# Kernel tuning notes

Hardware: AMD Instinct MI355X
Metric: run time of the kernel (lower is better)

Reference implementation:

```python
import jax, jax.numpy as jnp
import numpy as np

B, S, T, K = 96, 4, 16, 36           # groups, fixed 4 slots, max tags per slot, num boxes
V_DIM, Q_DIM, H = 1024, 512, 512


def setup_inputs() -> dict:
    key = jax.random.key(0)
    k_v, k_q, k_m, k_w1, k_b1, k_w2, k_b2 = jax.random.split(key, 7)

    # deterministic ragged lengths in [1, T], cyclic -> sum is exact
    lengths = (np.arange(B * S) % T) + 1              # [B*S], sum = 24 * 136 = 3264
    N = int(lengths.sum())                            # total rows in v / q
    # binary tag-attention mask: first `len` positions set per slot
    tags_attention = (np.arange(T)[None, :] < lengths[:, None]).astype(np.int32)
    tags_attention = jnp.asarray(tags_attention.reshape(B, S, T))

    v = jax.random.normal(k_v, (N, K, V_DIM), dtype=jnp.float32)
    q = jax.random.normal(k_q, (N, Q_DIM), dtype=jnp.float32)

    # box mask: random 0/1 but guarantee at least one valid box per group
    box_mask = (jax.random.uniform(k_m, (B, K)) < 0.9).astype(jnp.float32)
    box_mask = box_mask.at[:, 0].set(1.0)

    # FCNet (weight-normed Linear + ReLU; dropout inactive at eval) and scoring Linear
    w1 = jax.random.normal(k_w1, (V_DIM + Q_DIM, H), dtype=jnp.float32) * 0.02
    b1 = jax.random.normal(k_b1, (H,), dtype=jnp.float32) * 0.02
    w2 = jax.random.normal(k_w2, (H,), dtype=jnp.float32) * 0.02
    b2 = jax.random.normal(k_b2, (), dtype=jnp.float32) * 0.02

    return {"v": v, "q": q, "box_mask": box_mask, "tags_attention": tags_attention,
            "w1": w1, "b1": b1, "w2": w2, "b2": b2}


def reference(v, q, box_mask, tags_attention, w1, b1, w2, b2):
    N, Kb, _ = v.shape
    # logits: concat(v, q repeated over boxes) -> ReLU FC -> scalar score per box
    vq = jnp.concatenate([v, jnp.broadcast_to(q[:, None, :], (N, Kb, q.shape[-1]))], axis=-1)
    joint = jax.nn.relu(jnp.einsum('nkd,dh->nkh', vq, w1) + b1)      # [N, K, H]
    logits = jnp.einsum('nkh,h->nk', joint, w2) + b2                 # [N, K]

    # pad_sequence: ragged rows -> [B, S, T, K] via vectorized gather
    Bg, Sg, Tg = tags_attention.shape
    lengths = tags_attention.sum(-1).reshape(-1)                     # [B*S]
    starts = jnp.cumsum(lengths) - lengths                           # exclusive cumsum
    idx = starts[:, None] + jnp.arange(Tg)                           # [B*S, T]
    valid = jnp.arange(Tg)[None, :] < lengths[:, None]               # [B*S, T]
    gathered = jnp.take(logits, jnp.clip(idx, 0, N - 1), axis=0)     # [B*S, T, K]
    padded = jnp.where(valid[..., None], gathered, 0.0).reshape(Bg, Sg, Tg, Kb)

    # masked_softmax (allennlp-style) over the box dim with box_mask [B,1,1,K]
    mask = box_mask[:, None, None, :]
    s = jax.nn.softmax(padded * mask, axis=-1) * mask
    w = s / (s.sum(axis=-1, keepdims=True) + 1e-13)
    return w
```

## Files before the change

### kernel.cpp

```cpp
#include <hip/hip_runtime.h>
#include <hip/hip_bf16.h>
#include <cstdint>
#include <cstddef>

#define BB 96
#define SS 4
#define TT 16
#define KK 36
#define VDIM 1024
#define QDIM 512
#define HH 512
#define W1R 1536
#define NROWS 3264
#define MM (NROWS * KK)

typedef __attribute__((ext_vector_type(8))) short short8;
typedef __attribute__((ext_vector_type(4))) float f32x4;

static __device__ __forceinline__ unsigned short f2bf(float f) {
    union { float f; unsigned u; } v; v.f = f;
    unsigned u = v.u;
    u += 0x7FFFu + ((u >> 16) & 1u);
    return (unsigned short)(u >> 16);
}

static __device__ __forceinline__ unsigned pk2(float lo, float hi) {
    __hip_bfloat162 h = __float22bfloat162_rn(make_float2(lo, hi));
    union { __hip_bfloat162 h; unsigned u; } cv;
    cv.h = h;
    return cv.u;
}

__device__ __forceinline__ void gload_lds16(const void* g, void* l) {
    __builtin_amdgcn_global_load_lds(
        (const __attribute__((address_space(1))) unsigned int*)g,
        (__attribute__((address_space(3))) unsigned int*)l, 16, 0, 0);
}

#define SB() __builtin_amdgcn_sched_barrier(0)

__global__ __launch_bounds__(256) void prep_w1T(const float* __restrict__ w1,
                                                unsigned short* __restrict__ w1T) {
    int k = blockIdx.x * 256 + threadIdx.x;
    int c = blockIdx.y;
    w1T[(size_t)c * W1R + k] = f2bf(w1[(size_t)k * HH + c]);
}

__global__ __launch_bounds__(512) void starts_kernel(const int* __restrict__ tags,
                                                     int* __restrict__ starts,
                                                     int* __restrict__ lengths) {
    __shared__ int sl[BB * SS];
    int tid = threadIdx.x;
    int len = 0;
    if (tid < BB * SS) {
#pragma unroll
        for (int i = 0; i < TT; ++i) len += tags[tid * TT + i];
        sl[tid] = len;
    }
    __syncthreads();
    for (int off = 1; off < BB * SS; off <<= 1) {
        int v = 0;
        if (tid < BB * SS && tid >= off) v = sl[tid - off];
        __syncthreads();
        if (tid < BB * SS) sl[tid] += v;
        __syncthreads();
    }
    if (tid < BB * SS) { starts[tid] = sl[tid] - len; lengths[tid] = len; }
}

__global__ __launch_bounds__(256, 3) void qproj_mfma(const float* __restrict__ q,
                                                     const unsigned short* __restrict__ w1T,
                                                     const float* __restrict__ b1,
                                                     float* __restrict__ qp) {
    __shared__ __align__(16) unsigned short At[2][64 * 64];
    __shared__ __align__(16) unsigned short Bt[2][128 * 64];

    int tid = threadIdx.x, lane = tid & 63, wid = tid >> 6;
    int wm = wid >> 1, wn = wid & 1;
    int bx = blockIdx.x;
    int nb = bx & 3, mb = bx >> 2;
    int n0q = mb * 64, cb = nb * 128;
    int lr = lane & 15, lg = lane >> 4;

    const float* a_base = q + (size_t)(n0q + wid * 16 + (lane >> 4)) * QDIM + (lane & 15) * 4;
    const unsigned short* b_base = w1T + (size_t)(cb + wid * 32 + (lane >> 3)) * W1R + 1024
                                 + (((lane & 7) ^ (lane >> 3)) * 8);

    f32x4 acc[2][4];
#pragma unroll
    for (int mt = 0; mt < 2; ++mt)
#pragma unroll
        for (int nt = 0; nt < 4; ++nt) acc[mt][nt] = (f32x4){0.f, 0.f, 0.f, 0.f};

#define QP_CVT_WRITE(DST, AR)                                                  \
    _Pragma("unroll") for (int p = 0; p < 4; ++p) {                            \
        int r = wid * 16 + (lane >> 4) + p * 4;                                \
        int boff = r * 128 + ((((lane & 15) * 8)) ^ ((r & 7) << 4));           \
        uint2 d;                                                               \
        d.x = pk2(AR[p].x, AR[p].y);                                           \
        d.y = pk2(AR[p].z, AR[p].w);                                           \
        *(uint2*)((char*)(DST) + boff) = d;                                    \
    }

#define QP_COMPUTE(AC, BC)                                                     \
    _Pragma("unroll") for (int kk = 0; kk < 2; ++kk) {                         \
        short8 af[2], bf[4];                                                   \
        _Pragma("unroll") for (int mt = 0; mt < 2; ++mt) {                     \
            int R = wm * 32 + mt * 16 + lr;                                    \
            int off = R * 128 + ((kk * 64 + lg * 16) ^ ((R & 7) << 4));        \
            af[mt] = *(const short8*)((const char*)(AC) + off);                \
        }                                                                      \
        _Pragma("unroll") for (int nt = 0; nt < 4; ++nt) {                     \
            int R = wn * 64 + nt * 16 + lr;                                    \
            int off = R * 128 + ((kk * 64 + lg * 16) ^ ((R & 7) << 4));        \
            bf[nt] = *(const short8*)((const char*)(BC) + off);                \
        }                                                                      \
        __builtin_amdgcn_s_setprio(1);                                         \
        _Pragma("unroll") for (int mt = 0; mt < 2; ++mt)                       \
            _Pragma("unroll") for (int nt = 0; nt < 4; ++nt)                   \
                acc[mt][nt] = __builtin_amdgcn_mfma_f32_16x16x32_bf16(         \
                    af[mt], bf[nt], acc[mt][nt], 0, 0, 0);                     \
        __builtin_amdgcn_s_setprio(0);                                         \
    }

    {
        float4 ar[4];
#pragma unroll
        for (int p = 0; p < 4; ++p) ar[p] = *(const float4*)(a_base + (size_t)p * 4 * QDIM);
#pragma unroll
        for (int o = 0; o < 4; ++o)
            gload_lds16(b_base + (size_t)o * 8 * W1R, &Bt[0][(wid * 32 + o * 8) * 64]);
        SB();
        QP_CVT_WRITE(&At[0][0], ar)
    }
#pragma unroll 1
    for (int t = 0; t < 7; ++t) {
        int k0 = (t + 1) * 64;
        const unsigned short* Ac = &At[t & 1][0];
        const unsigned short* Bc = &Bt[t & 1][0];
        unsigned short* An = &At[(t + 1) & 1][0];
        unsigned short* Bn = &Bt[(t + 1) & 1][0];
        float4 ar[4];
#pragma unroll
        for (int p = 0; p < 4; ++p)
            ar[p] = *(const float4*)(a_base + (size_t)p * 4 * QDIM + k0);
#pragma unroll
        for (int o = 0; o < 4; ++o)
            gload_lds16(b_base + (size_t)o * 8 * W1R + k0, &Bn[(wid * 32 + o * 8) * 64]);
        SB();
        asm volatile("s_waitcnt vmcnt(8)" ::: "memory");
        asm volatile("s_waitcnt lgkmcnt(0)" ::: "memory");
        __builtin_amdgcn_s_barrier();
        SB();
        QP_COMPUTE(Ac, Bc)
        SB();
        QP_CVT_WRITE(An, ar)
    }
    SB();
    asm volatile("s_waitcnt vmcnt(0)" ::: "memory");
    asm volatile("s_waitcnt lgkmcnt(0)" ::: "memory");
    __builtin_amdgcn_s_barrier();
    SB();
    QP_COMPUTE(&At[1][0], &Bt[1][0])
#undef QP_COMPUTE
#undef QP_CVT_WRITE

#pragma unroll
    for (int nt = 0; nt < 4; ++nt) {
        int c = cb + wn * 64 + nt * 16 + lr;
        float b1v = b1[c];
#pragma unroll
        for (int mt = 0; mt < 2; ++mt)
#pragma unroll
            for (int r = 0; r < 4; ++r) {
                int row = wm * 32 + mt * 16 + lg * 4 + r;
                qp[(size_t)(n0q + row) * HH + c] = acc[mt][nt][r] + b1v;
            }
    }
}

__global__ __launch_bounds__(512, 4) void main_gemm(const float* __restrict__ v,
                                                    const unsigned short* __restrict__ w1T,
                                                    const float* __restrict__ qp,
                                                    const float* __restrict__ w2,
                                                    float* __restrict__ logits2) {
    __shared__ __align__(16) unsigned short At[128 * 64];
    __shared__ __align__(16) unsigned short Bt[2][256 * 64];

    int tid = threadIdx.x, lane = tid & 63, wid = tid >> 6;
    int wm = wid >> 2, wn = wid & 3;
    int bx = blockIdx.x;
    int xcd = bx & 7;
    int base = (xcd < 4) ? xcd * 230 : 920 + (xcd - 4) * 229;
    int orig = base + (bx >> 3);
    int ch = orig & 1, mb = orig >> 1;
    int m0 = mb * 128, cb = ch * 256;
    int lr = lane & 15, lg = lane >> 4;

    const float* a_base = v + (size_t)(m0 + wid * 16 + (lane >> 2)) * VDIM + (lane & 3) * 4;
    const unsigned short* b_base = w1T + (size_t)(cb + wid * 32 + (lane >> 3)) * W1R
                                 + (((lane & 7) ^ (lane >> 3)) * 8);

    f32x4 acc[4][4];
#pragma unroll
    for (int mt = 0; mt < 4; ++mt)
#pragma unroll
        for (int nt = 0; nt < 4; ++nt) acc[mt][nt] = (f32x4){0.f, 0.f, 0.f, 0.f};

#define MG_CVT_WRITE(AR)                                                       \
    _Pragma("unroll") for (int p = 0; p < 4; ++p) {                            \
        int r = wid * 16 + (lane >> 2);                                        \
        int boff = r * 128 + (((p * 32) + (lane & 3) * 8) ^ ((r & 7) << 4));   \
        uint2 d;                                                               \
        d.x = pk2(AR[p].x, AR[p].y);                                           \
        d.y = pk2(AR[p].z, AR[p].w);                                           \
        *(uint2*)((char*)&At[0] + boff) = d;                                   \
    }

#define MG_READ_A(AF, KKC)                                                     \
    _Pragma("unroll") for (int mt = 0; mt < 4; ++mt) {                         \
        int R = wm * 64 + mt * 16 + lr;                                        \
        int off = R * 128 + (((KKC) * 64 + lg * 16) ^ ((R & 7) << 4));         \
        AF[mt] = *(const short8*)((const char*)&At[0] + off);                  \
    }

#define MG_READ_B(BF, BC, KKC)                                                 \
    _Pragma("unroll") for (int nt = 0; nt < 4; ++nt) {                         \
        int C = wn * 64 + nt * 16 + lr;                                        \
        int off = C * 128 + (((KKC) * 64 + lg * 16) ^ ((C & 7) << 4));         \
        BF[nt] = *(const short8*)((const char*)(BC) + off);                    \
    }

#define MG_MFMA(AF, BF)                                                        \
    __builtin_amdgcn_s_setprio(1);                                             \
    _Pragma("unroll") for (int mt = 0; mt < 4; ++mt)                           \
        _Pragma("unroll") for (int nt = 0; nt < 4; ++nt)                       \
            acc[mt][nt] = __builtin_amdgcn_mfma_f32_16x16x32_bf16(             \
                AF[mt], BF[nt], acc[mt][nt], 0, 0, 0);                         \
    __builtin_amdgcn_s_setprio(0);

    {
#pragma unroll
        for (int o = 0; o < 4; ++o)
            gload_lds16(b_base + (size_t)o * 8 * W1R, &Bt[0][(wid * 32 + o * 8) * 64]);
        float4 ar[4];
#pragma unroll
        for (int p = 0; p < 4; ++p) ar[p] = *(const float4*)(a_base + p * 16);
        SB();
        MG_CVT_WRITE(ar)
    }

#pragma unroll 1
    for (int t = 0; t < 16; ++t) {
        int kA = (t < 15) ? (t + 1) * 64 : 960;
        const unsigned short* Bc = &Bt[t & 1][0];
        unsigned short* Bn = &Bt[(t + 1) & 1][0];
        float4 ar[4];
#pragma unroll
        for (int p = 0; p < 4; ++p)
            ar[p] = *(const float4*)(a_base + kA + p * 16);
        SB();
        asm volatile("s_waitcnt vmcnt(4)" ::: "memory");
        asm volatile("s_waitcnt lgkmcnt(0)" ::: "memory");
        __builtin_amdgcn_s_barrier();
        SB();
        if (t < 15) {
#pragma unroll
            for (int o = 0; o < 4; ++o)
                gload_lds16(b_base + (size_t)o * 8 * W1R + kA, Bn + (wid * 32 + o * 8) * 64);
        }
        SB();
        {
            short8 af0[4], bf0[4];
            MG_READ_A(af0, 0)
            MG_READ_B(bf0, Bc, 0)
            MG_MFMA(af0, bf0)
        }
        {
            short8 af1[4], bf1[4];
            MG_READ_A(af1, 1)
            MG_READ_B(bf1, Bc, 1)
            MG_MFMA(af1, bf1)
        }
        SB();
        asm volatile("s_waitcnt lgkmcnt(0)" ::: "memory");
        __builtin_amdgcn_s_barrier();
        SB();
        if (t < 15) { MG_CVT_WRITE(ar) }
    }
#undef MG_MFMA
#undef MG_READ_A
#undef MG_READ_B
#undef MG_CVT_WRITE

    __syncthreads();
    float* qs = (float*)&At[0];
    float* fl = qs + 5 * 256;
    int n0 = m0 / KK;
    for (int i = tid; i < 5 * 256; i += 512) {
        int nn = n0 + (i >> 8);
        if (nn >= NROWS) nn = NROWS - 1;
        qs[i] = qp[(size_t)nn * HH + cb + (i & 255)];
    }
    __syncthreads();

    float part[4][4] = {{0.f}};
#pragma unroll
    for (int nt = 0; nt < 4; ++nt) {
        int c = wn * 64 + nt * 16 + lr;
        float w2v = w2[cb + c];
#pragma unroll
        for (int mt = 0; mt < 4; ++mt)
#pragma unroll
            for (int r = 0; r < 4; ++r) {
                int row = wm * 64 + mt * 16 + lg * 4 + r;
                int ni = (m0 + row) / KK - n0;
                float pre = acc[mt][nt][r] + qs[ni * 256 + c];
                part[mt][r] += fmaxf(pre, 0.f) * w2v;
            }
    }
#pragma unroll
    for (int mt = 0; mt < 4; ++mt)
#pragma unroll
        for (int r = 0; r < 4; ++r) {
            float s = part[mt][r];
            s += __shfl_xor(s, 1, 64);
            s += __shfl_xor(s, 2, 64);
            s += __shfl_xor(s, 4, 64);
            s += __shfl_xor(s, 8, 64);
            if (lr == 0) fl[wn * 128 + wm * 64 + mt * 16 + lg * 4 + r] = s;
        }
    __syncthreads();
    if (tid < 128)
        logits2[(size_t)ch * MM + m0 + tid] =
            fl[tid] + fl[128 + tid] + fl[256 + tid] + fl[384 + tid];
}

__global__ __launch_bounds__(256) void softmax_kernel(const float* __restrict__ logits2,
                                                      const float* __restrict__ box_mask,
                                                      const int* __restrict__ starts,
                                                      const int* __restrict__ lengths,
                                                      float* __restrict__ out) {
    int lane = threadIdx.x & 63;
    int g = blockIdx.x * 4 + (threadIdx.x >> 6);
    int t   = g & (TT - 1);
    int row = g >> 4;
    int b   = row >> 2;

    int length = lengths[row];
    int start  = starts[row];

    int k = lane;
    bool kv = k < KK;
    float mval = kv ? box_mask[b * KK + k] : 0.f;
    bool act = kv && (mval != 0.f);

    float l = 0.f;
    if (act && t < length) {
        size_t idx = (size_t)(start + t) * KK + k;
        l = logits2[idx] + logits2[MM + idx];
    }

    float lm = act ? l : -1e30f;
#pragma unroll
    for (int off = 32; off >= 1; off >>= 1) lm = fmaxf(lm, __shfl_xor(lm, off, 64));

    float e = act ? expf(l - lm) : 0.f;
    float se = e;
#pragma unroll
    for (int off = 32; off >= 1; off >>= 1) se += __shfl_xor(se, off, 64);

    if (kv) out[(size_t)g * KK + k] = e / se;
}

extern "C" void kernel_launch(void* const* d_in, const int* in_sizes, int n_in,
                              void* d_out, int out_size, void* d_ws, size_t ws_size,
                              hipStream_t stream) {
    const float* v        = (const float*)d_in[0];
    const float* q        = (const float*)d_in[1];
    const float* box_mask = (const float*)d_in[2];
    const int*   tags     = (const int*)d_in[3];
    const float* w1       = (const float*)d_in[4];
    const float* b1       = (const float*)d_in[5];
    const float* w2       = (const float*)d_in[6];

    char* ws = (char*)d_ws;
    unsigned short* w1T   = (unsigned short*)ws;
    float* qp      = (float*)(ws + 1572864);
    float* logits2 = (float*)(ws + 1572864 + 6684672);
    int*   starts  = (int*)(ws + 1572864 + 6684672 + 940032);
    int*   lengths = (int*)(ws + 1572864 + 6684672 + 940032 + 1536);
    float* out     = (float*)d_out;

    hipLaunchKernelGGL(prep_w1T, dim3(6, 512), dim3(256), 0, stream, w1, w1T);
    hipLaunchKernelGGL(starts_kernel, dim3(1), dim3(512), 0, stream, tags, starts, lengths);
    hipLaunchKernelGGL(qproj_mfma, dim3((NROWS / 64) * 4), dim3(256), 0, stream,
                       q, w1T, b1, qp);
    hipLaunchKernelGGL(main_gemm, dim3((MM / 128) * 2), dim3(512), 0, stream,
                       v, w1T, qp, w2, logits2);
    hipLaunchKernelGGL(softmax_kernel, dim3((BB * SS * TT) / 4), dim3(256), 0, stream,
                       logits2, box_mask, starts, lengths, out);
}
```

Before: 263.6 us.

## Double main GEMM M-tile to 256 with double-buffered A and tiled w1 transpose

Each block of the main GEMM now covers 256 rows instead of 128. A is double-buffered in LDS, so one barrier per K-step is removed, and the loop is manually unrolled by two to alternate buffers. The larger tile halves the number of times W1 is reloaded and reuses each B fragment across 8 M-subtiles, at the cost of more accumulator registers (occupancy drops to 2 blocks per CU) and fewer blocks (918). The w1 transpose prep kernel now goes through a shared-memory tile so both its global reads and writes are coalesced.

Measured after the change: 252.4 us. 1.04x faster.

```diff
diff --git a/kernel.cpp b/kernel.cpp
--- a/kernel.cpp
+++ b/kernel.cpp
@@ -41,9 +41,20 @@
 
 __global__ __launch_bounds__(256) void prep_w1T(const float* __restrict__ w1,
                                                 unsigned short* __restrict__ w1T) {
-    int k = blockIdx.x * 256 + threadIdx.x;
-    int c = blockIdx.y;
-    w1T[(size_t)c * W1R + k] = f2bf(w1[(size_t)k * HH + c]);
+    __shared__ float tile[64][65];
+    int k0 = blockIdx.x * 64;
+    int c0 = blockIdx.y * 64;
+    int li = threadIdx.x & 63;
+    int gi = threadIdx.x >> 6;
+#pragma unroll
+    for (int r = 0; r < 64; r += 4)
+        tile[r + gi][li] = w1[(size_t)(k0 + r + gi) * HH + c0 + li];
+    __syncthreads();
+#pragma unroll
+    for (int r = 0; r < 64; r += 4) {
+        int c = r + gi;
+        w1T[(size_t)(c0 + c) * W1R + k0 + li] = f2bf(tile[li][c]);
+    }
 }
 
 __global__ __launch_bounds__(512) void starts_kernel(const int* __restrict__ tags,
@@ -179,148 +190,155 @@
     }
 }
 
-__global__ __launch_bounds__(512, 4) void main_gemm(const float* __restrict__ v,
+__global__ __launch_bounds__(512, 2) void main_gemm(const float* __restrict__ v,
                                                     const unsigned short* __restrict__ w1T,
                                                     const float* __restrict__ qp,
                                                     const float* __restrict__ w2,
                                                     float* __restrict__ logits2) {
-    __shared__ __align__(16) unsigned short At[128 * 64];
-    __shared__ __align__(16) unsigned short Bt[2][256 * 64];
+    __shared__ __align__(16) unsigned short At[2][16384];
+    __shared__ __align__(16) unsigned short Bt[2][16384];
 
     int tid = threadIdx.x, lane = tid & 63, wid = tid >> 6;
     int wm = wid >> 2, wn = wid & 3;
     int bx = blockIdx.x;
     int xcd = bx & 7;
-    int base = (xcd < 4) ? xcd * 230 : 920 + (xcd - 4) * 229;
+    int base = (xcd < 6) ? xcd * 115 : 690 + (xcd - 6) * 114;
     int orig = base + (bx >> 3);
     int ch = orig & 1, mb = orig >> 1;
-    int m0 = mb * 128, cb = ch * 256;
+    int m0 = mb * 256, cb = ch * 256;
     int lr = lane & 15, lg = lane >> 4;
 
-    const float* a_base = v + (size_t)(m0 + wid * 16 + (lane >> 2)) * VDIM + (lane & 3) * 4;
+    const float* a_base = v + (size_t)(m0 + wid * 32 + (lane >> 4)) * VDIM + (lane & 15) * 4;
     const unsigned short* b_base = w1T + (size_t)(cb + wid * 32 + (lane >> 3)) * W1R
                                  + (((lane & 7) ^ (lane >> 3)) * 8);
 
-    f32x4 acc[4][4];
-#pragma unroll
-    for (int mt = 0; mt < 4; ++mt)
+    f32x4 acc[8][4];
+#pragma unroll
+    for (int mt = 0; mt < 8; ++mt)
 #pragma unroll
         for (int nt = 0; nt < 4; ++nt) acc[mt][nt] = (f32x4){0.f, 0.f, 0.f, 0.f};
 
-#define MG_CVT_WRITE(AR)                                                       \
-    _Pragma("unroll") for (int p = 0; p < 4; ++p) {                            \
-        int r = wid * 16 + (lane >> 2);                                        \
-        int boff = r * 128 + (((p * 32) + (lane & 3) * 8) ^ ((r & 7) << 4));   \
+#define MG_CVT_WRITE(AN, AR)                                                   \
+    _Pragma("unroll") for (int p = 0; p < 8; ++p) {                            \
+        int r = wid * 32 + (lane >> 4) + p * 4;                                \
+        int boff = r * 128 + ((((lane & 15) * 8)) ^ ((r & 7) << 4));           \
         uint2 d;                                                               \
         d.x = pk2(AR[p].x, AR[p].y);                                           \
         d.y = pk2(AR[p].z, AR[p].w);                                           \
-        *(uint2*)((char*)&At[0] + boff) = d;                                   \
-    }
-
-#define MG_READ_A(AF, KKC)                                                     \
-    _Pragma("unroll") for (int mt = 0; mt < 4; ++mt) {                         \
-        int R = wm * 64 + mt * 16 + lr;                                        \
-        int off = R * 128 + (((KKC) * 64 + lg * 16) ^ ((R & 7) << 4));         \
-        AF[mt] = *(const short8*)((const char*)&At[0] + off);                  \
-    }
-
-#define MG_READ_B(BF, BC, KKC)                                                 \
-    _Pragma("unroll") for (int nt = 0; nt < 4; ++nt) {                         \
-        int C = wn * 64 + nt * 16 + lr;                                        \
-        int off = C * 128 + (((KKC) * 64 + lg * 16) ^ ((C & 7) << 4));         \
-        BF[nt] = *(const short8*)((const char*)(BC) + off);                    \
-    }
-
-#define MG_MFMA(AF, BF)                                                        \
+        *(uint2*)((char*)(AN) + boff) = d;                                     \
+    }
+
+#define MG_READ_A8(AF, AC, MTB)                                                \
+    _Pragma("unroll") for (int mt = 0; mt < 4; ++mt)                           \
+        _Pragma("unroll") for (int kk = 0; kk < 2; ++kk) {                     \
+            int R = wm * 128 + ((MTB) + mt) * 16 + lr;                         \
+            int off = R * 128 + ((kk * 64 + lg * 16) ^ ((R & 7) << 4));        \
+            AF[mt * 2 + kk] = *(const short8*)((const char*)(AC) + off);       \
+        }
+
+#define MG_READ_B8(BF, BC)                                                     \
+    _Pragma("unroll") for (int nt = 0; nt < 4; ++nt)                           \
+        _Pragma("unroll") for (int kk = 0; kk < 2; ++kk) {                     \
+            int C = wn * 64 + nt * 16 + lr;                                    \
+            int off = C * 128 + ((kk * 64 + lg * 16) ^ ((C & 7) << 4));        \
+            BF[nt * 2 + kk] = *(const short8*)((const char*)(BC) + off);       \
+        }
+
+#define MG_MFMA32(AF, BF, MTB)                                                 \
     __builtin_amdgcn_s_setprio(1);                                             \
     _Pragma("unroll") for (int mt = 0; mt < 4; ++mt)                           \
         _Pragma("unroll") for (int nt = 0; nt < 4; ++nt)                       \
-            acc[mt][nt] = __builtin_amdgcn_mfma_f32_16x16x32_bf16(             \
-                AF[mt], BF[nt], acc[mt][nt], 0, 0, 0);                         \
+            _Pragma("unroll") for (int kk = 0; kk < 2; ++kk)                   \
+                acc[(MTB) + mt][nt] = __builtin_amdgcn_mfma_f32_16x16x32_bf16( \
+                    AF[mt * 2 + kk], BF[nt * 2 + kk], acc[(MTB) + mt][nt],     \
+                    0, 0, 0);                                                  \
     __builtin_amdgcn_s_setprio(0);
 
+#define BODY(T, AC, AN, BC, BN, VM)                                            \
+  do {                                                                         \
+    float4 ar[8];                                                              \
+    if ((T) < 15) {                                                            \
+        const int kA = ((T) + 1) * 64;                                         \
+        _Pragma("unroll") for (int p = 0; p < 8; ++p)                          \
+            ar[p] = *(const float4*)(a_base + (size_t)p * 4 * VDIM + kA);      \
+    }                                                                          \
+    SB();                                                                      \
+    asm volatile("s_waitcnt vmcnt(" VM ")" ::: "memory");     \
+    asm volatile("s_waitcnt lgkmcnt(0)" ::: "memory");    \
+    __builtin_amdgcn_s_barrier();                                              \
+    SB();                                                                      \
+    if ((T) < 15) {       \
+        const int kB = ((T) + 1) * 64;                                         \
+        _Pragma("unroll") for (int o = 0; o < 4; ++o)                          \
+            gload_lds16(b_base + (size_t)o * 8 * W1R + kB,                     \
+                        (BN) + (wid * 32 + o * 8) * 64);                       \
+    }                                                                          \
+    SB();                                                                      \
+    {                                                                          \
+        short8 af0[8], bfv[8];                                                 \
+        MG_READ_A8(af0, AC, 0)                                                 \
+        MG_READ_B8(bfv, BC)                                                    \
+        MG_MFMA32(af0, bfv, 0)                                                 \
+        short8 af1[8];                                                         \
+        MG_READ_A8(af1, AC, 4)                                                 \
+        MG_MFMA32(af1, bfv, 4)                                                 \
+    }                                                                          \
+    SB();                                                                      \
+    if ((T) < 15) { MG_CVT_WRITE(AN, ar) }         \
+  } while (0)
+
     {
+        float4 ar[8];
+#pragma unroll
+        for (int p = 0; p < 8; ++p) ar[p] = *(const float4*)(a_base + (size_t)p * 4 * VDIM);
 #pragma unroll
         for (int o = 0; o < 4; ++o)
             gload_lds16(b_base + (size_t)o * 8 * W1R, &Bt[0][(wid * 32 + o * 8) * 64]);
-        float4 ar[4];
-#pragma unroll
-        for (int p = 0; p < 4; ++p) ar[p] = *(const float4*)(a_base + p * 16);
         SB();
-        MG_CVT_WRITE(ar)
+        MG_CVT_WRITE(At[0], ar)
     }
 
 #pragma unroll 1
-    for (int t = 0; t < 16; ++t) {
-        int kA = (t < 15) ? (t + 1) * 64 : 960;
-        const unsigned short* Bc = &Bt[t & 1][0];
-        unsigned short* Bn = &Bt[(t + 1) & 1][0];
-        float4 ar[4];
-#pragma unroll
-        for (int p = 0; p < 4; ++p)
-            ar[p] = *(const float4*)(a_base + kA + p * 16);
-        SB();
-        asm volatile("s_waitcnt vmcnt(4)" ::: "memory");
-        asm volatile("s_waitcnt lgkmcnt(0)" ::: "memory");
-        __builtin_amdgcn_s_barrier();
-        SB();
-        if (t < 15) {
-#pragma unroll
-            for (int o = 0; o < 4; ++o)
-                gload_lds16(b_base + (size_t)o * 8 * W1R + kA, Bn + (wid * 32 + o * 8) * 64);
-        }
-        SB();
-        {
-            short8 af0[4], bf0[4];
-            MG_READ_A(af0, 0)
-            MG_READ_B(bf0, Bc, 0)
-            MG_MFMA(af0, bf0)
-        }
-        {
-            short8 af1[4], bf1[4];
-            MG_READ_A(af1, 1)
-            MG_READ_B(bf1, Bc, 1)
-            MG_MFMA(af1, bf1)
-        }
-        SB();
-        asm volatile("s_waitcnt lgkmcnt(0)" ::: "memory");
-        __builtin_amdgcn_s_barrier();
-        SB();
-        if (t < 15) { MG_CVT_WRITE(ar) }
-    }
-#undef MG_MFMA
-#undef MG_READ_A
-#undef MG_READ_B
+    for (int tt = 0; tt < 14; tt += 2) {
+        BODY(tt,     At[0], At[1], Bt[0], Bt[1], "8");
+        BODY(tt + 1, At[1], At[0], Bt[1], Bt[0], "8");
+    }
+    BODY(14, At[0], At[1], Bt[0], Bt[1], "8");
+    BODY(15, At[1], At[0], Bt[1], Bt[0], "0");
+#undef BODY
+#undef MG_MFMA32
+#undef MG_READ_A8
+#undef MG_READ_B8
 #undef MG_CVT_WRITE
 
     __syncthreads();
-    float* qs = (float*)&At[0];
-    float* fl = qs + 5 * 256;
+    float* qs = (float*)&At[0][0];
+    float* fl = qs + 9 * 256;
     int n0 = m0 / KK;
-    for (int i = tid; i < 5 * 256; i += 512) {
+    for (int i = tid; i < 9 * 256; i += 512) {
         int nn = n0 + (i >> 8);
         if (nn >= NROWS) nn = NROWS - 1;
         qs[i] = qp[(size_t)nn * HH + cb + (i & 255)];
     }
     __syncthreads();
 
-    float part[4][4] = {{0.f}};
+    float part[8][4] = {{0.f}};
 #pragma unroll
     for (int nt = 0; nt < 4; ++nt) {
         int c = wn * 64 + nt * 16 + lr;
         float w2v = w2[cb + c];
 #pragma unroll
-        for (int mt = 0; mt < 4; ++mt)
+        for (int mt = 0; mt < 8; ++mt)
 #pragma unroll
             for (int r = 0; r < 4; ++r) {
-                int row = wm * 64 + mt * 16 + lg * 4 + r;
+                int row = wm * 128 + mt * 16 + lg * 4 + r;
                 int ni = (m0 + row) / KK - n0;
                 float pre = acc[mt][nt][r] + qs[ni * 256 + c];
                 part[mt][r] += fmaxf(pre, 0.f) * w2v;
             }
     }
 #pragma unroll
-    for (int mt = 0; mt < 4; ++mt)
+    for (int mt = 0; mt < 8; ++mt)
 #pragma unroll
         for (int r = 0; r < 4; ++r) {
             float s = part[mt][r];
@@ -328,12 +346,12 @@
             s += __shfl_xor(s, 2, 64);
             s += __shfl_xor(s, 4, 64);
             s += __shfl_xor(s, 8, 64);
-            if (lr == 0) fl[wn * 128 + wm * 64 + mt * 16 + lg * 4 + r] = s;
+            if (lr == 0) fl[wn * 256 + wm * 128 + mt * 16 + lg * 4 + r] = s;
         }
     __syncthreads();
-    if (tid < 128)
+    if (tid < 256)
         logits2[(size_t)ch * MM + m0 + tid] =
-            fl[tid] + fl[128 + tid] + fl[256 + tid] + fl[384 + tid];
+            fl[tid] + fl[256 + tid] + fl[512 + tid] + fl[768 + tid];
 }
 
 __global__ __launch_bounds__(256) void softmax_kernel(const float* __restrict__ logits2,
@@ -392,11 +410,11 @@
     int*   lengths = (int*)(ws + 1572864 + 6684672 + 940032 + 1536);
     float* out     = (float*)d_out;
 
-    hipLaunchKernelGGL(prep_w1T, dim3(6, 512), dim3(256), 0, stream, w1, w1T);
+    hipLaunchKernelGGL(prep_w1T, dim3(24, 8), dim3(256), 0, stream, w1, w1T);
     hipLaunchKernelGGL(starts_kernel, dim3(1), dim3(512), 0, stream, tags, starts, lengths);
     hipLaunchKernelGGL(qproj_mfma, dim3((NROWS / 64) * 4), dim3(256), 0, stream,
                        q, w1T, b1, qp);
-    hipLaunchKernelGGL(main_gemm, dim3((MM / 128) * 2), dim3(512), 0, stream,
+    hipLaunchKernelGGL(main_gemm, dim3((MM / 256) * 2), dim3(512), 0, stream,
                        v, w1T, qp, w2, logits2);
     hipLaunchKernelGGL(softmax_kernel, dim3((BB * SS * TT) / 4), dim3(256), 0, stream,
                        logits2, box_mask, starts, lengths, out);
```
